# Optimization experiments

Hardware: AMD Instinct MI355X
Metric: run time of the kernel (lower is better)

The kernel has to match this reference:

```python
import jax, jax.numpy as jnp
import numpy as np
from jax import lax

# dims
B, T, D = 2, 1024, 512
H, K, V = 8, 64, 64      # head_k_dim = head_v_dim = 64
CONV = 4
# IVON / module hyperparams (from __init__ defaults)
LR, B1, B2, WD, LAM = 1e-3, 0.9, 0.999, 0.0, 1.0
EPS = 1e-5               # RMSNorm eps
SCALE = K ** -0.5


def _silu(x):
    return x * jax.nn.sigmoid(x)


def _short_conv(x, w):
    """Causal depthwise conv1d (kernel_size=CONV, no bias) + SiLU. x:[B,T,C], w:[C,CONV]."""
    xp = jnp.pad(x, ((0, 0), (CONV - 1, 0), (0, 0)))
    y = sum(xp[:, i:i + x.shape[1]] * w[:, i] for i in range(CONV))
    return _silu(y)


def _l2norm(x):
    return x * lax.rsqrt(jnp.sum(x * x, -1, keepdims=True) + 1e-6)


def setup_inputs() -> dict:
    key = jax.random.key(0)
    ks = jax.random.split(key, 10)
    s = 0.02
    return {
        "hidden_states": jax.random.normal(ks[0], (B, T, D), jnp.float32),
        "Wq": jax.random.normal(ks[1], (D, H * K), jnp.float32) * s,
        "Wk": jax.random.normal(ks[2], (D, H * K), jnp.float32) * s,
        "Wv": jax.random.normal(ks[3], (D, H * V), jnp.float32) * s,
        "Wb": jax.random.normal(ks[4], (D, H), jnp.float32) * s,
        "cw_q": jax.random.normal(ks[5], (H * K, CONV), jnp.float32) * 0.5,
        "cw_k": jax.random.normal(ks[6], (H * K, CONV), jnp.float32) * 0.5,
        "cw_v": jax.random.normal(ks[7], (H * V, CONV), jnp.float32) * 0.5,
        "rms_w": jnp.ones((V,), jnp.float32),
        "Wo": jax.random.normal(ks[8], (H * V, D), jnp.float32) * s,
    }


def reference(hidden_states, Wq, Wk, Wv, Wb, cw_q, cw_k, cw_v, rms_w, Wo):
    x = hidden_states
    # projections -> causal depthwise short conv (+SiLU, qk_activation='silu')
    q = _short_conv(x @ Wq, cw_q).reshape(B, T, H, K)
    k = _short_conv(x @ Wk, cw_k).reshape(B, T, H, K)
    v = _short_conv(x @ Wv, cw_v).reshape(B, T, H, V)
    beta = jax.nn.sigmoid(x @ Wb)                     # [B,T,H]
    # qk l2-norm inside kernel (qk_norm='l2'), scale on q
    q = _l2norm(q) * SCALE
    k = _l2norm(k)

    # fused recurrent IVON delta-rule: per-step outer-product gradient of
    # 0.5||k @ S - v||^2, momentum g, diag preconditioner h (noise-free IVON).
    def step(carry, inp):
        S, h, g = carry                               # each [B,H,K,V]
        qt, kt, vt, bt = inp                          # [B,H,K],[B,H,K],[B,H,V],[B,H]
        pred = jnp.einsum('bhk,bhkv->bhv', kt, S)
        grad = kt[..., None] * (pred - vt)[..., None, :]   # [B,H,K,V]
        g = B1 * g + (1.0 - B1) * grad
        h = B2 * h + (1.0 - B2) * grad * grad
        S = S - LR * bt[..., None, None] * (g + WD * S) / (h + LAM)
        o = jnp.einsum('bhk,bhkv->bhv', qt, S)
        return (S, h, g), o

    z = jnp.zeros((B, H, K, V), jnp.float32)
    inps = (jnp.swapaxes(q, 0, 1), jnp.swapaxes(k, 0, 1),
            jnp.swapaxes(v, 0, 1), jnp.swapaxes(beta, 0, 1))
    _, o = lax.scan(step, (z, z, z), inps)            # o: [T,B,H,V]
    o = jnp.swapaxes(o, 0, 1)                          # [B,T,H,V]

    # RMSNorm over head_v_dim, then output projection
    o = o * lax.rsqrt(jnp.mean(o * o, -1, keepdims=True) + EPS) * rms_w
    o = o.reshape(B, T, H * V) @ Wo                    # [B,T,D]
    return o
```

## Files before the change

### kernel.cpp

```cpp
#include <hip/hip_runtime.h>
#include <hip/hip_bf16.h>
#include <math.h>

#define Bb 2
#define Tt 1024
#define Dd 512
#define Hh 8
#define Kk 64
#define Vv 64
#define BT (Bb*Tt)
#define HK (Hh*Kk)

#define B1c 0.9f
#define B2c 0.999f
#define LRc 1e-3f
#define SCALEc 0.125f

typedef short s8v __attribute__((ext_vector_type(8)));
typedef float f4v __attribute__((ext_vector_type(4)));

__device__ __forceinline__ unsigned short f2bf(float x) {
  unsigned u = __float_as_uint(x);
  u += 0x7FFFu + ((u >> 16) & 1u);
  return (unsigned short)(u >> 16);
}
__device__ __forceinline__ float bf2f(unsigned short h) {
  return __uint_as_float((unsigned)h << 16);
}

template <int CTRL>
__device__ __forceinline__ float dpp_add(float v) {
  int y = __builtin_amdgcn_update_dpp(0, __float_as_int(v), CTRL, 0xF, 0xF, true);
  return v + __int_as_float(y);
}

typedef unsigned uint2_t __attribute__((ext_vector_type(2)));

__device__ __forceinline__ float xor16_add(float x) {
#if __has_builtin(__builtin_amdgcn_permlane16_swap)
  uint2_t r = __builtin_amdgcn_permlane16_swap(__float_as_uint(x), __float_as_uint(x),
                                               false, false);
  return __uint_as_float(r.x) + __uint_as_float(r.y);
#else
  int y = __builtin_amdgcn_ds_swizzle(__float_as_int(x), 0x401F);
  return x + __int_as_float(y);
#endif
}

__device__ __forceinline__ float xor32_add(float x) {
#if __has_builtin(__builtin_amdgcn_permlane32_swap)
  uint2_t r = __builtin_amdgcn_permlane32_swap(__float_as_uint(x), __float_as_uint(x),
                                               false, false);
  return __uint_as_float(r.x) + __uint_as_float(r.y);
#else
  return x + __shfl_xor(x, 32, 64);
#endif
}

__device__ __forceinline__ float reduce16(float x) {
  x = dpp_add<0xB1>(x);
  x = dpp_add<0x4E>(x);
  x = dpp_add<0x141>(x);
  x = dpp_add<0x140>(x);
  return x;
}

__device__ __forceinline__ float reduce64(float x) {
  x = reduce16(x);
  x = xor16_add(x);
  x = xor32_add(x);
  return x;
}

__global__ __launch_bounds__(256) void cvt_x_kernel(
    const float* __restrict__ x, unsigned short* __restrict__ hi,
    unsigned short* __restrict__ lo) {
  const int i = (blockIdx.x * 256 + threadIdx.x) * 8;
  float4 a = *(const float4*)(x + i);
  float4 b = *(const float4*)(x + i + 4);
  const float v[8] = {a.x, a.y, a.z, a.w, b.x, b.y, b.z, b.w};
  union { unsigned short u[8]; uint4 q; } ph, pl;
#pragma unroll
  for (int j = 0; j < 8; ++j) {
    unsigned short h = f2bf(v[j]);
    ph.u[j] = h;
    pl.u[j] = f2bf(v[j] - bf2f(h));
  }
  *(uint4*)(hi + i) = ph.q;
  *(uint4*)(lo + i) = pl.q;
}

__global__ __launch_bounds__(256) void cvt_w_kernel(
    const float* __restrict__ W0, const float* __restrict__ W1,
    const float* __restrict__ W2,
    unsigned short* __restrict__ hib, unsigned short* __restrict__ lob) {
  __shared__ float Ts[64][65];
  const int z = blockIdx.z;
  const float* W = (z == 0) ? W0 : (z == 1) ? W1 : W2;
  unsigned short* hi = hib + (size_t)z * 512 * 512;
  unsigned short* lo = lob + (size_t)z * 512 * 512;
  const int tk = blockIdx.x * 64;
  const int tn = blockIdx.y * 64;
  const int r  = threadIdx.x >> 2;
  const int cg = threadIdx.x & 3;
#pragma unroll
  for (int j = 0; j < 4; ++j) {
    float4 v = *(const float4*)(W + (size_t)(tk + r) * 512 + tn + cg * 16 + j * 4);
    Ts[r][cg * 16 + j * 4 + 0] = v.x;
    Ts[r][cg * 16 + j * 4 + 1] = v.y;
    Ts[r][cg * 16 + j * 4 + 2] = v.z;
    Ts[r][cg * 16 + j * 4 + 3] = v.w;
  }
  __syncthreads();
  union { unsigned short u[16]; uint4 q[2]; } ph, pl;
#pragma unroll
  for (int j = 0; j < 16; ++j) {
    float v = Ts[cg * 16 + j][r];
    unsigned short h = f2bf(v);
    ph.u[j] = h;
    pl.u[j] = f2bf(v - bf2f(h));
  }
  const size_t ob = (size_t)(tn + r) * 512 + tk + cg * 16;
  *(uint4*)(hi + ob) = ph.q[0];
  *(uint4*)(hi + ob + 8) = ph.q[1];
  *(uint4*)(lo + ob) = pl.q[0];
  *(uint4*)(lo + ob + 8) = pl.q[1];
}

__device__ __forceinline__ void gemm_mfma_body(
    const unsigned short* __restrict__ Ahi, const unsigned short* __restrict__ Alo,
    const unsigned short* __restrict__ Bhi, const unsigned short* __restrict__ Blo,
    float* __restrict__ C) {
  __shared__ unsigned short Ah[64][40], Al[64][40], Bh[64][40], Bl[64][40];
  const int tid = threadIdx.x;
  const int bm = blockIdx.x * 64;
  const int bn = blockIdx.y * 64;
  const int srow = tid >> 2;
  const int skoff = (tid & 3) * 8;
  const int l = tid & 63, w = tid >> 6;
  const int arow = (l & 15) + 16 * w;
  const int koff = (l >> 4) * 8;

  const unsigned short* pAh = Ahi + (size_t)(bm + srow) * 512 + skoff;
  const unsigned short* pAl = Alo + (size_t)(bm + srow) * 512 + skoff;
  const unsigned short* pBh = Bhi + (size_t)(bn + srow) * 512 + skoff;
  const unsigned short* pBl = Blo + (size_t)(bn + srow) * 512 + skoff;

  f4v acc0 = {0.f, 0.f, 0.f, 0.f}, acc1 = acc0, acc2 = acc0, acc3 = acc0;

  uint4 rah = *(const uint4*)(pAh);
  uint4 ral = *(const uint4*)(pAl);
  uint4 rbh = *(const uint4*)(pBh);
  uint4 rbl = *(const uint4*)(pBl);

  for (int k0 = 0; k0 < 512; k0 += 32) {
    __syncthreads();
    *(uint4*)&Ah[srow][skoff] = rah;
    *(uint4*)&Al[srow][skoff] = ral;
    *(uint4*)&Bh[srow][skoff] = rbh;
    *(uint4*)&Bl[srow][skoff] = rbl;
    __syncthreads();
    if (k0 + 32 < 512) {
      rah = *(const uint4*)(pAh + k0 + 32);
      ral = *(const uint4*)(pAl + k0 + 32);
      rbh = *(const uint4*)(pBh + k0 + 32);
      rbl = *(const uint4*)(pBl + k0 + 32);
    }
    const s8v ah = *(const s8v*)&Ah[arow][koff];
    const s8v al = *(const s8v*)&Al[arow][koff];
#pragma unroll
    for (int c = 0; c < 4; ++c) {
      const s8v bh = *(const s8v*)&Bh[16 * c + (l & 15)][koff];
      const s8v bl = *(const s8v*)&Bl[16 * c + (l & 15)][koff];
      f4v* acc = (c == 0) ? &acc0 : (c == 1) ? &acc1 : (c == 2) ? &acc2 : &acc3;
      *acc = __builtin_amdgcn_mfma_f32_16x16x32_bf16(al, bh, *acc, 0, 0, 0);
      *acc = __builtin_amdgcn_mfma_f32_16x16x32_bf16(ah, bl, *acc, 0, 0, 0);
      *acc = __builtin_amdgcn_mfma_f32_16x16x32_bf16(ah, bh, *acc, 0, 0, 0);
    }
  }

  const int crow = bm + 16 * w + (l >> 4) * 4;
  const int ccol = bn + (l & 15);
#pragma unroll
  for (int i = 0; i < 4; ++i) {
    C[(size_t)(crow + i) * 512 + ccol + 0]  = acc0[i];
    C[(size_t)(crow + i) * 512 + ccol + 16] = acc1[i];
    C[(size_t)(crow + i) * 512 + ccol + 32] = acc2[i];
    C[(size_t)(crow + i) * 512 + ccol + 48] = acc3[i];
  }
}

__global__ __launch_bounds__(256) void gemm3_mfma_kernel(
    const unsigned short* __restrict__ xhi, const unsigned short* __restrict__ xlo,
    const unsigned short* __restrict__ whi, const unsigned short* __restrict__ wlo,
    float* __restrict__ qp, float* __restrict__ kp, float* __restrict__ vp) {
  const int z = blockIdx.z;
  float* Cp = (z == 0) ? qp : (z == 1) ? kp : vp;
  gemm_mfma_body(xhi, xlo, whi + (size_t)z * 512 * 512, wlo + (size_t)z * 512 * 512, Cp);
}

__global__ __launch_bounds__(256) void gemm1_mfma_kernel(
    const unsigned short* __restrict__ ahi, const unsigned short* __restrict__ alo,
    const unsigned short* __restrict__ whi, const unsigned short* __restrict__ wlo,
    float* __restrict__ C) {
  gemm_mfma_body(ahi, alo, whi, wlo, C);
}

__global__ __launch_bounds__(256) void beta_kernel(const float* __restrict__ x,
                                                   const float* __restrict__ Wb,
                                                   float* __restrict__ beta) {
  int gid = blockIdx.x * blockDim.x + threadIdx.x;
  int bt = gid >> 3, h = gid & 7;
  const float4* xr = (const float4*)(x + (size_t)bt * Dd);
  float s = 0.f;
#pragma unroll 4
  for (int d4 = 0; d4 < Dd / 4; ++d4) {
    float4 xv = xr[d4];
    const float* wb = Wb + (d4 * 4) * Hh + h;
    s = fmaf(xv.x, wb[0 * Hh], s);
    s = fmaf(xv.y, wb[1 * Hh], s);
    s = fmaf(xv.z, wb[2 * Hh], s);
    s = fmaf(xv.w, wb[3 * Hh], s);
  }
  beta[gid] = 1.f / (1.f + expf(-s));
}

__global__ __launch_bounds__(256) void conv_kernel(
    const float* __restrict__ qp, const float* __restrict__ kp,
    const float* __restrict__ vp,
    const float* __restrict__ cwq, const float* __restrict__ cwk,
    const float* __restrict__ cwv,
    float* __restrict__ qc, float* __restrict__ kc, float* __restrict__ vc) {
  const int mode = blockIdx.z;
  const float* pre; const float* cw; float* post;
  if (mode == 0)      { pre = qp; cw = cwq; post = qc; }
  else if (mode == 1) { pre = kp; cw = cwk; post = kc; }
  else                { pre = vp; cw = cwv; post = vc; }

  const int idx = blockIdx.x * 4 + (threadIdx.x >> 6);
  const int lane = threadIdx.x & 63;
  const int b = idx >> 13;
  const int th = idx & 8191;
  const int t = th >> 3;
  const int h = th & 7;
  const int ch = h * 64 + lane;

  float y = 0.f;
#pragma unroll
  for (int i = 0; i < 4; ++i) {
    int tt = t + i - 3;
    if (tt >= 0)
      y += pre[((size_t)(b * Tt + tt)) * HK + ch] * cw[ch * 4 + i];
  }
  y = y / (1.f + expf(-y));
  if (mode < 2) {
    float ss = reduce64(y * y);
    y *= rsqrtf(ss + 1e-6f);
    if (mode == 0) y *= SCALEc;
  }
  post[((size_t)(b * Tt + t)) * HK + ch] = y;
}

#define TC 16

__global__ __launch_bounds__(256) void scan_kernel(
    const float* __restrict__ qc, const float* __restrict__ kc,
    const float* __restrict__ vc, const float* __restrict__ beta,
    float* __restrict__ o) {
  __shared__ float ks[2][TC][64];
  __shared__ float qs[2][TC][64];
  __shared__ float2 vb[2][TC][4];

  const int tid  = threadIdx.x;
  const int lane = tid & 63;
  const int w    = tid >> 6;
  const int bid  = blockIdx.x;
  const int vq   = bid >> 4;
  const int bh   = bid & 15;
  const int b = bh >> 3, h = bh & 7;
  const int v  = vq * 4 + w;

  const size_t base2 = ((size_t)b * Tt) * HK + h * 64;
  const float* bp = beta + ((size_t)b * Tt) * Hh + h;
  float* op = o + base2 + v;

  const int sr = tid >> 4;
  const int sg = tid & 15;
  const int vr = tid >> 2;
  const int vcc = tid & 3;

  {
    float4 k4 = *(const float4*)(kc + base2 + (size_t)sr * HK + sg * 4);
    float4 q4 = *(const float4*)(qc + base2 + (size_t)sr * HK + sg * 4);
    *(float4*)&ks[0][sr][sg * 4] = k4;
    *(float4*)&qs[0][sr][sg * 4] = q4;
    if (tid < 64) {
      float vv = vc[base2 + (size_t)vr * HK + vq * 4 + vcc];
      float lb = (0.1f * LRc) * bp[(size_t)vr * Hh];
      vb[0][vr][vcc] = make_float2(vv, lb);
    }
    __syncthreads();
  }

  float S = 0.f, G = 0.f, H = 0.f, r = 1.f;

  for (int tile = 0; tile < Tt / TC; ++tile) {
    const int d = tile & 1;
    const int t0 = tile * TC;
    const int more = (tile + 1 < Tt / TC);
    const int tn = more ? t0 + TC : t0;

    float4 nk = *(const float4*)(kc + base2 + (size_t)(tn + sr) * HK + sg * 4);
    float4 nq = *(const float4*)(qc + base2 + (size_t)(tn + sr) * HK + sg * 4);
    float nv = 0.f, nb = 0.f;
    if (tid < 64) {
      nv = vc[base2 + (size_t)(tn + vr) * HK + vq * 4 + vcc];
      nb = (0.1f * LRc) * bp[(size_t)(tn + vr) * Hh];
    }

    float pred = reduce64(ks[d][0][lane] * S);

#pragma unroll
    for (int s = 0; s < TC; ++s) {
      const float kv = ks[d][s][lane];
      const float qv = qs[d][s][lane];
      const float2 vbc = vb[d][s][w];

      const float diff = pred - vbc.x;
      const float lrb = vbc.y;
      const float gr = kv * diff;
      G = fmaf(B1c, G, gr);
      H = fmaf(B2c, H, gr * gr);
      const float dd = fmaf(H, 0.001f, 1.0f);
      r = r * fmaf(-dd, r, 2.0f);
      S = fmaf(-lrb, G * r, S);

      float po = qv * S;
      if (s + 1 < TC) {
        float pp = ks[d][s + 1][lane] * S;
        po = dpp_add<0xB1>(po);   pp = dpp_add<0xB1>(pp);
        po = dpp_add<0x4E>(po);   pp = dpp_add<0x4E>(pp);
        po = dpp_add<0x141>(po);  pp = dpp_add<0x141>(pp);
        po = dpp_add<0x140>(po);  pp = dpp_add<0x140>(pp);
        po = xor16_add(po);       pp = xor16_add(pp);
        po = xor32_add(po);       pp = xor32_add(pp);
        pred = pp;
      } else {
        po = reduce64(po);
      }
      op[(size_t)(t0 + s) * HK] = po;
    }

    if (more) {
      *(float4*)&ks[d ^ 1][sr][sg * 4] = nk;
      *(float4*)&qs[d ^ 1][sr][sg * 4] = nq;
      if (tid < 64) vb[d ^ 1][vr][vcc] = make_float2(nv, nb);
    }
    __syncthreads();
  }
}

__global__ __launch_bounds__(256) void rmsnorm_kernel(
    const float* __restrict__ o, const float* __restrict__ rmsw,
    unsigned short* __restrict__ hi, unsigned short* __restrict__ lo) {
  const int idx = blockIdx.x * 4 + (threadIdx.x >> 6);
  const int lane = threadIdx.x & 63;
  const float* p = o + (size_t)idx * 64;
  float y = p[lane];
  float ss = reduce64(y * y);
  y = y * rsqrtf(ss * (1.f / 64.f) + 1e-5f) * rmsw[lane];
  unsigned short h = f2bf(y);
  hi[(size_t)idx * 64 + lane] = h;
  lo[(size_t)idx * 64 + lane] = f2bf(y - bf2f(h));
}

extern "C" void kernel_launch(void* const* d_in, const int* in_sizes, int n_in,
                              void* d_out, int out_size, void* d_ws, size_t ws_size,
                              hipStream_t stream) {
  const float* x    = (const float*)d_in[0];
  const float* Wq   = (const float*)d_in[1];
  const float* Wk   = (const float*)d_in[2];
  const float* Wv   = (const float*)d_in[3];
  const float* Wb   = (const float*)d_in[4];
  const float* cwq  = (const float*)d_in[5];
  const float* cwk  = (const float*)d_in[6];
  const float* cwv  = (const float*)d_in[7];
  const float* rmsw = (const float*)d_in[8];
  const float* Wo   = (const float*)d_in[9];
  float* out = (float*)d_out;
  float* ws  = (float*)d_ws;

  const size_t SZ = (size_t)BT * HK;
  float* qp   = ws;
  float* kp   = ws + 1 * SZ;
  float* vp   = ws + 2 * SZ;
  float* qc   = ws + 3 * SZ;
  float* kc   = ws + 4 * SZ;
  float* vc   = ws + 5 * SZ;
  float* beta = ws + 6 * SZ;
  float* on   = qp;

  unsigned short* xhi  = (unsigned short*)qc;
  unsigned short* xlo  = xhi + SZ;
  unsigned short* wh3  = (unsigned short*)kc;
  unsigned short* wl3  = wh3 + 3 * 512 * 512;
  unsigned short* wohi = (unsigned short*)vc;
  unsigned short* wolo = wohi + 512 * 512;
  unsigned short* onhi = (unsigned short*)kp;
  unsigned short* onlo = (unsigned short*)vp;

  cvt_x_kernel<<<dim3(BT * Dd / (256 * 8)), 256, 0, stream>>>(x, xhi, xlo);
  cvt_w_kernel<<<dim3(8, 8, 3), 256, 0, stream>>>(Wq, Wk, Wv, wh3, wl3);
  gemm3_mfma_kernel<<<dim3(BT / 64, HK / 64, 3), 256, 0, stream>>>(
      xhi, xlo, wh3, wl3, qp, kp, vp);
  beta_kernel<<<dim3(BT * Hh / 256), 256, 0, stream>>>(x, Wb, beta);
  conv_kernel<<<dim3(Bb * Tt * Hh / 4, 1, 3), 256, 0, stream>>>(
      qp, kp, vp, cwq, cwk, cwv, qc, kc, vc);
  scan_kernel<<<dim3(Bb * Hh * (Vv / 4)), 256, 0, stream>>>(
      qc, kc, vc, beta, on);
  cvt_w_kernel<<<dim3(8, 8, 1), 256, 0, stream>>>(Wo, Wo, Wo, wohi, wolo);
  rmsnorm_kernel<<<dim3(Bb * Tt * Hh / 4), 256, 0, stream>>>(on, rmsw, onhi, onlo);
  gemm1_mfma_kernel<<<dim3(BT / 64, HK / 64, 1), 256, 0, stream>>>(
      onhi, onlo, wohi, wolo, out);
}
```

Baseline: 208.1 us.

## Process two value columns per wavefront in scan using packed FP32 math

Each wavefront in the recurrent scan kernel now tracks two value columns instead of one. The state updates use packed two-wide FMA vectors, and four DPP reductions are interleaved to expose more instruction-level parallelism. This halves the grid from 256 to 128 blocks and makes the output stores two floats wide. The aim is to hide the latency of the serial reduction chain and cut redundant k/q loads, at the cost of fewer concurrent blocks on a GPU with many CUs.

```diff
diff --git a/kernel.cpp b/kernel.cpp
--- a/kernel.cpp
+++ b/kernel.cpp
@@ -18,6 +18,7 @@
 
 typedef short s8v __attribute__((ext_vector_type(8)));
 typedef float f4v __attribute__((ext_vector_type(4)));
+typedef float f2v __attribute__((ext_vector_type(2)));
 
 __device__ __forceinline__ unsigned short f2bf(float x) {
   unsigned u = __float_as_uint(x);
@@ -263,13 +264,18 @@
 
 #define TC 16
 
+__device__ __forceinline__ f2v pk_fma(f2v a, f2v b, f2v c) {
+  return __builtin_elementwise_fma(a, b, c);
+}
+
 __global__ __launch_bounds__(256) void scan_kernel(
     const float* __restrict__ qc, const float* __restrict__ kc,
     const float* __restrict__ vc, const float* __restrict__ beta,
     float* __restrict__ o) {
   __shared__ float ks[2][TC][64];
   __shared__ float qs[2][TC][64];
-  __shared__ float2 vb[2][TC][4];
+  __shared__ float vs[2][TC][8];
+  __shared__ float lr[2][TC];
 
   const int tid  = threadIdx.x;
   const int lane = tid & 63;
@@ -278,31 +284,30 @@
   const int vq   = bid >> 4;
   const int bh   = bid & 15;
   const int b = bh >> 3, h = bh & 7;
-  const int v  = vq * 4 + w;
+  const int colbase = vq * 8;
+  const int v0 = colbase + 2 * w;
 
   const size_t base2 = ((size_t)b * Tt) * HK + h * 64;
   const float* bp = beta + ((size_t)b * Tt) * Hh + h;
-  float* op = o + base2 + v;
+  float* op = o + base2 + v0;
 
   const int sr = tid >> 4;
   const int sg = tid & 15;
-  const int vr = tid >> 2;
-  const int vcc = tid & 3;
 
   {
     float4 k4 = *(const float4*)(kc + base2 + (size_t)sr * HK + sg * 4);
     float4 q4 = *(const float4*)(qc + base2 + (size_t)sr * HK + sg * 4);
     *(float4*)&ks[0][sr][sg * 4] = k4;
     *(float4*)&qs[0][sr][sg * 4] = q4;
-    if (tid < 64) {
-      float vv = vc[base2 + (size_t)vr * HK + vq * 4 + vcc];
-      float lb = (0.1f * LRc) * bp[(size_t)vr * Hh];
-      vb[0][vr][vcc] = make_float2(vv, lb);
-    }
+    if (sg < 8) vs[0][sr][sg] = vc[base2 + (size_t)sr * HK + colbase + sg];
+    if (tid < TC) lr[0][tid] = (0.1f * LRc) * bp[(size_t)tid * Hh];
     __syncthreads();
   }
 
-  float S = 0.f, G = 0.f, H = 0.f, r = 1.f;
+  f2v S = {0.f, 0.f}, G = S, H = S;
+  f2v r = {1.f, 1.f};
+  const f2v c_b1 = {B1c, B1c}, c_b2 = {B2c, B2c};
+  const f2v c_em3 = {0.001f, 0.001f}, c_one = {1.f, 1.f}, c_two = {2.f, 2.f};
 
   for (int tile = 0; tile < Tt / TC; ++tile) {
     const int d = tile & 1;
@@ -312,49 +317,72 @@
 
     float4 nk = *(const float4*)(kc + base2 + (size_t)(tn + sr) * HK + sg * 4);
     float4 nq = *(const float4*)(qc + base2 + (size_t)(tn + sr) * HK + sg * 4);
-    float nv = 0.f, nb = 0.f;
-    if (tid < 64) {
-      nv = vc[base2 + (size_t)(tn + vr) * HK + vq * 4 + vcc];
-      nb = (0.1f * LRc) * bp[(size_t)(tn + vr) * Hh];
+    float  nv = (sg < 8) ? vc[base2 + (size_t)(tn + sr) * HK + colbase + sg] : 0.f;
+    float  nb = (tid < TC) ? (0.1f * LRc) * bp[(size_t)(tn + tid) * Hh] : 0.f;
+
+    f2v pred;
+    {
+      const float k0v = ks[d][0][lane];
+      float ax = k0v * S.x, ay = k0v * S.y;
+      ax = dpp_add<0xB1>(ax);   ay = dpp_add<0xB1>(ay);
+      ax = dpp_add<0x4E>(ax);   ay = dpp_add<0x4E>(ay);
+      ax = dpp_add<0x141>(ax);  ay = dpp_add<0x141>(ay);
+      ax = dpp_add<0x140>(ax);  ay = dpp_add<0x140>(ay);
+      ax = xor16_add(ax);       ay = xor16_add(ay);
+      ax = xor32_add(ax);       ay = xor32_add(ay);
+      pred.x = ax; pred.y = ay;
     }
-
-    float pred = reduce64(ks[d][0][lane] * S);
 
 #pragma unroll
     for (int s = 0; s < TC; ++s) {
       const float kv = ks[d][s][lane];
       const float qv = qs[d][s][lane];
-      const float2 vbc = vb[d][s][w];
-
-      const float diff = pred - vbc.x;
-      const float lrb = vbc.y;
-      const float gr = kv * diff;
-      G = fmaf(B1c, G, gr);
-      H = fmaf(B2c, H, gr * gr);
-      const float dd = fmaf(H, 0.001f, 1.0f);
-      r = r * fmaf(-dd, r, 2.0f);
-      S = fmaf(-lrb, G * r, S);
-
-      float po = qv * S;
+      const f2v vv = *(const f2v*)&vs[d][s][2 * w];
+      const float lrb = lr[d][s];
+
+      const f2v kv2 = {kv, kv};
+      const f2v diff = pred - vv;
+      const f2v gr = kv2 * diff;
+      G = pk_fma(c_b1, G, gr);
+      H = pk_fma(c_b2, H, gr * gr);
+      const f2v dd = pk_fma(H, c_em3, c_one);
+      r = r * pk_fma(-dd, r, c_two);
+      const f2v lrb2 = {lrb, lrb};
+      S = pk_fma(-lrb2, G * r, S);
+
+      const f2v qv2 = {qv, qv};
+      f2v po = qv2 * S;
       if (s + 1 < TC) {
-        float pp = ks[d][s + 1][lane] * S;
-        po = dpp_add<0xB1>(po);   pp = dpp_add<0xB1>(pp);
-        po = dpp_add<0x4E>(po);   pp = dpp_add<0x4E>(pp);
-        po = dpp_add<0x141>(po);  pp = dpp_add<0x141>(pp);
-        po = dpp_add<0x140>(po);  pp = dpp_add<0x140>(pp);
-        po = xor16_add(po);       pp = xor16_add(pp);
-        po = xor32_add(po);       pp = xor32_add(pp);
-        pred = pp;
+        const float kn = ks[d][s + 1][lane];
+        const f2v kn2 = {kn, kn};
+        f2v pp = kn2 * S;
+        float a = po.x, bb = po.y, c = pp.x, e = pp.y;
+        a = dpp_add<0xB1>(a);  bb = dpp_add<0xB1>(bb);  c = dpp_add<0xB1>(c);  e = dpp_add<0xB1>(e);
+        a = dpp_add<0x4E>(a);  bb = dpp_add<0x4E>(bb);  c = dpp_add<0x4E>(c);  e = dpp_add<0x4E>(e);
+        a = dpp_add<0x141>(a); bb = dpp_add<0x141>(bb); c = dpp_add<0x141>(c); e = dpp_add<0x141>(e);
+        a = dpp_add<0x140>(a); bb = dpp_add<0x140>(bb); c = dpp_add<0x140>(c); e = dpp_add<0x140>(e);
+        a = xor16_add(a);      bb = xor16_add(bb);      c = xor16_add(c);      e = xor16_add(e);
+        a = xor32_add(a);      bb = xor32_add(bb);      c = xor32_add(c);      e = xor32_add(e);
+        po.x = a; po.y = bb;
+        pred.x = c; pred.y = e;
       } else {
-        po = reduce64(po);
+        float a = po.x, bb = po.y;
+        a = dpp_add<0xB1>(a);  bb = dpp_add<0xB1>(bb);
+        a = dpp_add<0x4E>(a);  bb = dpp_add<0x4E>(bb);
+        a = dpp_add<0x141>(a); bb = dpp_add<0x141>(bb);
+        a = dpp_add<0x140>(a); bb = dpp_add<0x140>(bb);
+        a = xor16_add(a);      bb = xor16_add(bb);
+        a = xor32_add(a);      bb = xor32_add(bb);
+        po.x = a; po.y = bb;
       }
-      op[(size_t)(t0 + s) * HK] = po;
+      *(float2*)(op + (size_t)(t0 + s) * HK) = make_float2(po.x, po.y);
     }
 
     if (more) {
       *(float4*)&ks[d ^ 1][sr][sg * 4] = nk;
       *(float4*)&qs[d ^ 1][sr][sg * 4] = nq;
-      if (tid < 64) vb[d ^ 1][vr][vcc] = make_float2(nv, nb);
+      if (sg < 8) vs[d ^ 1][sr][sg] = nv;
+      if (tid < TC) lr[d ^ 1][tid] = nb;
     }
     __syncthreads();
   }
@@ -416,7 +444,7 @@
   beta_kernel<<<dim3(BT * Hh / 256), 256, 0, stream>>>(x, Wb, beta);
   conv_kernel<<<dim3(Bb * Tt * Hh / 4, 1, 3), 256, 0, stream>>>(
       qp, kp, vp, cwq, cwk, cwv, qc, kc, vc);
-  scan_kernel<<<dim3(Bb * Hh * (Vv / 4)), 256, 0, stream>>>(
+  scan_kernel<<<dim3(Bb * Hh * (Vv / 8)), 256, 0, stream>>>(
       qc, kc, vc, beta, on);
   cvt_w_kernel<<<dim3(8, 8, 1), 256, 0, stream>>>(Wo, Wo, Wo, wohi, wolo);
   rmsnorm_kernel<<<dim3(Bb * Tt * Hh / 4), 256, 0, stream>>>(on, rmsw, onhi, onlo);
```

New measurement: 255.7 us. 1.23x slower.
